# Kernel tuning notes

Measured on AMD Instinct MI355X. Metric: run time of the kernel, lower is better.

The kernel has to match this reference:

```python
import jax, jax.numpy as jnp
import numpy as np

B, T, D, U = 32, 2048, 1024, 1024

def setup_inputs() -> dict:
    key = jax.random.key(0)
    ks = jax.random.split(key, 6)
    scale = 1.0 / np.sqrt(D)
    return {
        "features": jax.random.normal(ks[0], (B, T, D), dtype=jnp.float32),
        "hidden": jax.random.normal(ks[1], (B, D), dtype=jnp.float32),
        "W1": jax.random.normal(ks[2], (D, U), dtype=jnp.float32) * scale,
        "b1": jnp.zeros((U,), dtype=jnp.float32),
        "W2": jax.random.normal(ks[3], (D, U), dtype=jnp.float32) * scale,
        "b2": jnp.zeros((U,), dtype=jnp.float32),
        "V": jax.random.normal(ks[4], (U, 1), dtype=jnp.float32) * (1.0 / np.sqrt(U)),
        "bV": jnp.zeros((1,), dtype=jnp.float32),
    }

def reference(features, hidden, W1, b1, W2, b2, V, bV):
    # features: [B,T,D], hidden: [B,D]
    proj_f = jnp.einsum('btd,du->btu', features, W1) + b1          # [B,T,U]
    proj_h = (hidden @ W2 + b2)[:, None, :]                        # [B,1,U]
    score = jnp.tanh(proj_f + proj_h)                              # [B,T,U]
    logits = jnp.einsum('btu,uo->bto', score, V) + bV              # [B,T,1]
    attention_weights = jax.nn.softmax(logits, axis=1)             # [B,T,1]
    context_vector = jnp.sum(attention_weights * features, axis=1) # [B,D]
    return context_vector, attention_weights
```

## Files before the change

### kernel.cpp

```cpp
#include <hip/hip_runtime.h>
#include <hip/hip_bf16.h>
#include <hip/hip_fp16.h>

#define B_ 32
#define T_ 2048
#define D_ 1024
#define U_ 1024
#define M_ (B_ * T_)
#define NT_ 16

typedef _Float16 f16x8 __attribute__((ext_vector_type(8)));
typedef float f32x4 __attribute__((ext_vector_type(4)));

__device__ __forceinline__ float fast_tanh(float x) {
    float xc = fminf(fmaxf(x, -10.f), 10.f);
    float e = __expf(2.f * xc);
    return 1.f - 2.f / (e + 1.f);
}

__device__ __forceinline__ void load_lds16(const void* g, void* l) {
    __builtin_amdgcn_global_load_lds(
        (const __attribute__((address_space(1))) void*)g,
        (__attribute__((address_space(3))) void*)l, 16, 0, 0);
}

__global__ void precastT_kernel(const float* __restrict__ in,
                                _Float16* __restrict__ out) {
    __shared__ __align__(16) _Float16 lds[16 * 1024];
    int mt = blockIdx.x;
    int t = threadIdx.x;
    const float* src = in + (size_t)mt * 16384;
    #pragma unroll
    for (int i = 0; i < 4; ++i) {
        int o = (i * 256 + t) * 16;
        int r = o >> 10, c = o & 1023;
        f32x4 a0 = *(const f32x4*)(src + o);
        f32x4 a1 = *(const f32x4*)(src + o + 4);
        f32x4 a2 = *(const f32x4*)(src + o + 8);
        f32x4 a3 = *(const f32x4*)(src + o + 12);
        f16x8 h0, h1;
        h0[0]=(_Float16)a0[0]; h0[1]=(_Float16)a0[1]; h0[2]=(_Float16)a0[2]; h0[3]=(_Float16)a0[3];
        h0[4]=(_Float16)a1[0]; h0[5]=(_Float16)a1[1]; h0[6]=(_Float16)a1[2]; h0[7]=(_Float16)a1[3];
        h1[0]=(_Float16)a2[0]; h1[1]=(_Float16)a2[1]; h1[2]=(_Float16)a2[2]; h1[3]=(_Float16)a2[3];
        h1[4]=(_Float16)a3[0]; h1[5]=(_Float16)a3[1]; h1[6]=(_Float16)a3[2]; h1[7]=(_Float16)a3[3];
        int u0 = c >> 3, swz = r & 7;
        *(f16x8*)((char*)lds + r * 2048 + ((u0 ^ swz) << 4)) = h0;
        *(f16x8*)((char*)lds + r * 2048 + (((u0 + 1) ^ swz) << 4)) = h1;
    }
    __syncthreads();
    int slot = t & 15, kb0 = t >> 4, ssw = slot & 7;
    _Float16* dst = out + (size_t)mt * 16384 + slot * 8;
    #pragma unroll
    for (int i = 0; i < 8; ++i) {
        int kb = kb0 + i * 16;
        f16x8 h = *(const f16x8*)((char*)lds + slot * 2048 + ((kb ^ ssw) << 4));
        *(f16x8*)(dst + kb * 128) = h;
    }
}

__global__ void transpose_cast_W1T_kernel(const float* __restrict__ W1,
                                          _Float16* __restrict__ W1T) {
    int u = blockIdx.x * 256 + threadIdx.x;
    int d0 = blockIdx.y * 64;
    _Float16* dst = W1T + (size_t)(u >> 4) * 16384 + (u & 15) * 8;
    for (int j8 = 0; j8 < 8; ++j8) {
        f16x8 h;
        #pragma unroll
        for (int j = 0; j < 8; ++j)
            h[j] = (_Float16)W1[(size_t)(d0 + j8 * 8 + j) * U_ + u];
        *(f16x8*)(dst + (size_t)(d0 / 8 + j8) * 128) = h;
    }
}

__global__ void proj_h_partial_kernel(const float* __restrict__ hidden,
                                      const float* __restrict__ W2,
                                      float* __restrict__ pph) {
    int u = blockIdx.x * 256 + threadIdx.x;
    int c = blockIdx.y;
    __shared__ float hb[32][128];
    for (int i = threadIdx.x; i < 32 * 128; i += 256)
        hb[i >> 7][i & 127] = hidden[(i >> 7) * D_ + c * 128 + (i & 127)];
    __syncthreads();
    float acc[32] = {};
    for (int d = 0; d < 128; ++d) {
        float w = W2[(size_t)(c * 128 + d) * U_ + u];
        #pragma unroll
        for (int b = 0; b < 32; ++b) acc[b] = fmaf(hb[b][d], w, acc[b]);
    }
    #pragma unroll
    for (int b = 0; b < 32; ++b)
        pph[((size_t)c * 32 + b) * U_ + u] = acc[b];
}

__global__ void proj_h_combine_kernel(const float* __restrict__ pph,
                                      const float* __restrict__ b1,
                                      const float* __restrict__ b2,
                                      float* __restrict__ ph) {
    int u = blockIdx.x * 256 + threadIdx.x;
    float bias = b1[u] + b2[u];
    for (int b = 0; b < 32; ++b) {
        float s = bias;
        #pragma unroll
        for (int c = 0; c < 8; ++c) s += pph[((size_t)c * 32 + b) * U_ + u];
        ph[b * U_ + u] = s;
    }
}


#define LOAD_AF(dst, s) do { \
    const char* a_ = aT + (s) * 1024; \
    _Pragma("unroll") \
    for (int m_ = 0; m_ < 4; ++m_) \
        dst[m_] = *(const f16x8*)(a_ + (m_ << 15)); \
} while (0)

#define READ_BF(s) do { \
    _Pragma("unroll") \
    for (int n_ = 0; n_ < 4; ++n_) \
        bfc[n_] = *(const f16x8*)(lB + n_ * 32768 + (s) * 1024 + l16); \
} while (0)

#define MFMA_STEP(AF) do { \
    __builtin_amdgcn_s_setprio(1); \
    _Pragma("unroll") \
    for (int m_ = 0; m_ < 4; ++m_) \
        _Pragma("unroll") \
        for (int n_ = 0; n_ < 4; ++n_) \
            acc[m_][n_] = __builtin_amdgcn_mfma_f32_16x16x32_f16( \
                AF[m_], bfc[n_], acc[m_][n_], 0, 0, 0); \
    __builtin_amdgcn_s_setprio(0); \
} while (0)

__global__ __launch_bounds__(1024, 4)
void gemm_logits_v8_kernel(const _Float16* __restrict__ featT,
                           const _Float16* __restrict__ W1T,
                           const float* __restrict__ ph,
                           const float* __restrict__ V,
                           float* __restrict__ part)
{
    __shared__ __align__(16) _Float16 Bs[65536];

    int bid = blockIdx.x;
    int xcd = bid & 7, local = bid >> 3;
    int nt = local & 15;
    int mg = xcd * 8 + (local >> 4);

    int tid = threadIdx.x;
    int l = tid & 63, w = tid >> 6;
    int l16 = l * 16;
    const char* lB = (const char*)Bs;

    const char* aT = (const char*)featT + ((size_t)(mg * 64 + w * 4) << 15) + l16;

    {
        const char* src = (const char*)W1T + (size_t)nt * 131072;
        #pragma unroll
        for (int i = 0; i < 8; ++i)
            load_lds16(src + i * 16384 + tid * 16, (char*)Bs + i * 16384 + tid * 16);
    }

    f16x8 afA[4], afB[4], bfc[4];
    f32x4 acc[4][4] = {};

    LOAD_AF(afA, 0);

    float Vv[4];
    #pragma unroll
    for (int n = 0; n < 4; ++n) Vv[n] = V[nt * 64 + n * 16 + (l & 15)];

    asm volatile("s_waitcnt vmcnt(0)" ::: "memory");
    __builtin_amdgcn_s_barrier();

    #pragma unroll 1
    for (int s = 0; s < 32; s += 2) {
        READ_BF(s);
        LOAD_AF(afB, s + 1);
        MFMA_STEP(afA);
        READ_BF(s + 1);
        if (s < 30) LOAD_AF(afA, s + 2);
        MFMA_STEP(afB);
    }

    int row0 = mg * 1024 + w * 64;
    const float* phb = ph + (mg >> 1) * U_;
    float phv[4];
    #pragma unroll
    for (int n = 0; n < 4; ++n) phv[n] = phb[nt * 64 + n * 16 + (l & 15)];
    #pragma unroll
    for (int m = 0; m < 4; ++m) {
        #pragma unroll
        for (int r = 0; r < 4; ++r) {
            float p = 0.f;
            #pragma unroll
            for (int n = 0; n < 4; ++n)
                p = fmaf(fast_tanh(acc[m][n][r] + phv[n]), Vv[n], p);
            p += __shfl_xor(p, 1, 64);
            p += __shfl_xor(p, 2, 64);
            p += __shfl_xor(p, 4, 64);
            p += __shfl_xor(p, 8, 64);
            if ((l & 15) == 0)
                part[(size_t)nt * M_ + row0 + m * 16 + (l >> 4) * 4 + r] = p;
        }
    }
}

__global__ void softmax_kernel(const float* __restrict__ part,
                               float* __restrict__ wout) {
    int b = blockIdx.x;
    int tid = threadIdx.x;
    __shared__ float red[8];
    float lg[8];
    #pragma unroll
    for (int j = 0; j < 8; ++j) {
        int t = tid + j * 256;
        float s = 0.f;
        #pragma unroll
        for (int p = 0; p < NT_; ++p)
            s += part[(size_t)p * M_ + b * T_ + t];
        lg[j] = s;
    }
    float mx = lg[0];
    #pragma unroll
    for (int j = 1; j < 8; ++j) mx = fmaxf(mx, lg[j]);
    #pragma unroll
    for (int off = 1; off < 64; off <<= 1) mx = fmaxf(mx, __shfl_xor(mx, off, 64));
    int wv = tid >> 6;
    if ((tid & 63) == 0) red[wv] = mx;
    __syncthreads();
    mx = fmaxf(fmaxf(red[0], red[1]), fmaxf(red[2], red[3]));
    float e[8];
    float sum = 0.f;
    #pragma unroll
    for (int j = 0; j < 8; ++j) { e[j] = __expf(lg[j] - mx); sum += e[j]; }
    #pragma unroll
    for (int off = 1; off < 64; off <<= 1) sum += __shfl_xor(sum, off, 64);
    if ((tid & 63) == 0) red[4 + wv] = sum;
    __syncthreads();
    sum = red[4] + red[5] + red[6] + red[7];
    float inv = 1.f / sum;
    #pragma unroll
    for (int j = 0; j < 8; ++j)
        wout[b * T_ + tid + j * 256] = e[j] * inv;
}

__global__ void context_v7_kernel(const _Float16* __restrict__ featT,
                                  const float* __restrict__ w,
                                  float* __restrict__ ctx) {
    int b = blockIdx.x;
    int dc = blockIdx.y;
    int t = threadIdx.x;
    __shared__ float wLds[2048];
    for (int i = t; i < 2048; i += 256) wLds[i] = w[b * T_ + i];
    __syncthreads();

    float acc[8] = {};
    const char* base = (const char*)featT + (size_t)b * 128 * 32768 + dc * 4096 + t * 16;
    int slot = t & 15;
    #pragma unroll 4
    for (int mt = 0; mt < 128; ++mt) {
        f16x8 v = *(const f16x8*)(base + (size_t)mt * 32768);
        float wt = wLds[mt * 16 + slot];
        #pragma unroll
        for (int j = 0; j < 8; ++j) acc[j] = fmaf(wt, (float)v[j], acc[j]);
    }
    #pragma unroll
    for (int j = 0; j < 8; ++j) {
        acc[j] += __shfl_xor(acc[j], 1, 64);
        acc[j] += __shfl_xor(acc[j], 2, 64);
        acc[j] += __shfl_xor(acc[j], 4, 64);
        acc[j] += __shfl_xor(acc[j], 8, 64);
    }
    if ((t & 15) == 0) {
        float* o = ctx + b * D_ + dc * 128 + (t >> 4) * 8;
        #pragma unroll
        for (int j = 0; j < 8; ++j) o[j] = acc[j];
    }
}

extern "C" void kernel_launch(void* const* d_in, const int* in_sizes, int n_in,
                              void* d_out, int out_size, void* d_ws, size_t ws_size,
                              hipStream_t stream) {
    const float* features = (const float*)d_in[0];
    const float* hidden   = (const float*)d_in[1];
    const float* W1       = (const float*)d_in[2];
    const float* b1       = (const float*)d_in[3];
    const float* W2       = (const float*)d_in[4];
    const float* b2       = (const float*)d_in[5];
    const float* V        = (const float*)d_in[6];

    float* ctx_out = (float*)d_out;
    float* w_out   = ctx_out + B_ * D_;

    char* ws = (char*)d_ws;
    _Float16* W1T  = (_Float16*)ws;
    float* ph      = (float*)(ws + (size_t)(2 << 20));
    float* pph     = (float*)(ws + (size_t)(2 << 20) + (1 << 17));
    float* part    = (float*)(ws + (size_t)(4 << 20));
    _Float16* featT = (_Float16*)(ws + (size_t)(8 << 20));

    transpose_cast_W1T_kernel<<<dim3(4, 16), 256, 0, stream>>>(W1, W1T);
    proj_h_partial_kernel<<<dim3(4, 8), 256, 0, stream>>>(hidden, W2, pph);
    proj_h_combine_kernel<<<4, 256, 0, stream>>>(pph, b1, b2, ph);
    precastT_kernel<<<4096, 256, 0, stream>>>(features, featT);

    gemm_logits_v8_kernel<<<1024, 1024, 0, stream>>>(featT, W1T, ph, V, part);

    softmax_kernel<<<B_, 256, 0, stream>>>(part, w_out);
    context_v7_kernel<<<dim3(B_, 8), 256, 0, stream>>>(featT, w_out, ctx_out);
}
```

Before: 314.8 us.

## Switch logits GEMM to 32x32x16 MFMA with matching 32-row pre-swizzled layouts

Replaces the 16x16x32 MFMA tiling with 32x32x16 MFMA instructions, so each wave computes a 64x64 tile with 2x2 larger accumulators. The feature and W1 precast kernels are rewritten to emit a 32-row interleaved fp16 layout that the new fragment loads expect, and the context kernel is adapted to that layout. The main loop now double-buffers both A and B fragments and adds sched_barriers to fix the interleaving of loads and MFMAs. The intent is fewer MFMA issues and fewer fragment loads per FLOP. The cost is larger per-lane accumulator state, a changed epilogue reduction, and context-kernel access patterns that may be less efficient.

```diff
diff --git a/kernel.cpp b/kernel.cpp
--- a/kernel.cpp
+++ b/kernel.cpp
@@ -11,6 +11,7 @@
 
 typedef _Float16 f16x8 __attribute__((ext_vector_type(8)));
 typedef float f32x4 __attribute__((ext_vector_type(4)));
+typedef float f32x16 __attribute__((ext_vector_type(16)));
 
 __device__ __forceinline__ float fast_tanh(float x) {
     float xc = fminf(fmaxf(x, -10.f), 10.f);
@@ -26,35 +27,33 @@
 
 __global__ void precastT_kernel(const float* __restrict__ in,
                                 _Float16* __restrict__ out) {
-    __shared__ __align__(16) _Float16 lds[16 * 1024];
+    __shared__ __align__(16) _Float16 lds[32 * 1024];
     int mt = blockIdx.x;
     int t = threadIdx.x;
-    const float* src = in + (size_t)mt * 16384;
-    #pragma unroll
-    for (int i = 0; i < 4; ++i) {
-        int o = (i * 256 + t) * 16;
-        int r = o >> 10, c = o & 1023;
-        f32x4 a0 = *(const f32x4*)(src + o);
-        f32x4 a1 = *(const f32x4*)(src + o + 4);
-        f32x4 a2 = *(const f32x4*)(src + o + 8);
-        f32x4 a3 = *(const f32x4*)(src + o + 12);
-        f16x8 h0, h1;
-        h0[0]=(_Float16)a0[0]; h0[1]=(_Float16)a0[1]; h0[2]=(_Float16)a0[2]; h0[3]=(_Float16)a0[3];
-        h0[4]=(_Float16)a1[0]; h0[5]=(_Float16)a1[1]; h0[6]=(_Float16)a1[2]; h0[7]=(_Float16)a1[3];
-        h1[0]=(_Float16)a2[0]; h1[1]=(_Float16)a2[1]; h1[2]=(_Float16)a2[2]; h1[3]=(_Float16)a2[3];
-        h1[4]=(_Float16)a3[0]; h1[5]=(_Float16)a3[1]; h1[6]=(_Float16)a3[2]; h1[7]=(_Float16)a3[3];
-        int u0 = c >> 3, swz = r & 7;
-        *(f16x8*)((char*)lds + r * 2048 + ((u0 ^ swz) << 4)) = h0;
-        *(f16x8*)((char*)lds + r * 2048 + (((u0 + 1) ^ swz) << 4)) = h1;
-    }
-    __syncthreads();
-    int slot = t & 15, kb0 = t >> 4, ssw = slot & 7;
-    _Float16* dst = out + (size_t)mt * 16384 + slot * 8;
-    #pragma unroll
-    for (int i = 0; i < 8; ++i) {
-        int kb = kb0 + i * 16;
-        f16x8 h = *(const f16x8*)((char*)lds + slot * 2048 + ((kb ^ ssw) << 4));
-        *(f16x8*)(dst + kb * 128) = h;
+    const float* src = in + (size_t)mt * 32 * 1024;
+    #pragma unroll
+    for (int i = 0; i < 16; ++i) {
+        int idx = (i * 256 + t) * 8;
+        int row = idx >> 10, k = idx & 1023;
+        f32x4 a = *(const f32x4*)(src + idx);
+        f32x4 b = *(const f32x4*)(src + idx + 4);
+        f16x8 h;
+        h[0]=(_Float16)a[0]; h[1]=(_Float16)a[1]; h[2]=(_Float16)a[2]; h[3]=(_Float16)a[3];
+        h[4]=(_Float16)b[0]; h[5]=(_Float16)b[1]; h[6]=(_Float16)b[2]; h[7]=(_Float16)b[3];
+        int u = k >> 3;
+        *(f16x8*)((char*)lds + row * 2048 + ((u ^ (row & 15)) << 4)) = h;
+    }
+    __syncthreads();
+    char* dst = (char*)out + (size_t)mt * 65536;
+    #pragma unroll
+    for (int i = 0; i < 16; ++i) {
+        int o = i * 4096 + t * 16;
+        int k16 = o >> 10;
+        int l = (o >> 4) & 63;
+        int row = l & 31, khalf = l >> 5;
+        int u = k16 * 2 + khalf;
+        f16x8 h = *(const f16x8*)((char*)lds + row * 2048 + ((u ^ (row & 15)) << 4));
+        *(f16x8*)(dst + o) = h;
     }
 }
 
@@ -62,13 +61,15 @@
                                           _Float16* __restrict__ W1T) {
     int u = blockIdx.x * 256 + threadIdx.x;
     int d0 = blockIdx.y * 64;
-    _Float16* dst = W1T + (size_t)(u >> 4) * 16384 + (u & 15) * 8;
+    char* base = (char*)W1T + (size_t)(u >> 5) * 65536 + (u & 31) * 16;
     for (int j8 = 0; j8 < 8; ++j8) {
+        int k = d0 + j8 * 8;
         f16x8 h;
         #pragma unroll
         for (int j = 0; j < 8; ++j)
-            h[j] = (_Float16)W1[(size_t)(d0 + j8 * 8 + j) * U_ + u];
-        *(f16x8*)(dst + (size_t)(d0 / 8 + j8) * 128) = h;
+            h[j] = (_Float16)W1[(size_t)(k + j) * U_ + u];
+        int k16 = k >> 4, khalf = (k >> 3) & 1;
+        *(f16x8*)(base + k16 * 1024 + khalf * 512) = h;
     }
 }
 
@@ -107,33 +108,30 @@
 }
 
 
-#define LOAD_AF(dst, s) do { \
-    const char* a_ = aT + (s) * 1024; \
-    _Pragma("unroll") \
-    for (int m_ = 0; m_ < 4; ++m_) \
-        dst[m_] = *(const f16x8*)(a_ + (m_ << 15)); \
+#define SB0 __builtin_amdgcn_sched_barrier(0);
+
+#define LOAD_AF(dst, s16) do { \
+    dst[0] = *(const f16x8*)(aT + (s16) * 1024); \
+    dst[1] = *(const f16x8*)(aT + 65536 + (s16) * 1024); \
 } while (0)
 
-#define READ_BF(s) do { \
-    _Pragma("unroll") \
-    for (int n_ = 0; n_ < 4; ++n_) \
-        bfc[n_] = *(const f16x8*)(lB + n_ * 32768 + (s) * 1024 + l16); \
+#define READ_BF(dst, s16) do { \
+    dst[0] = *(const f16x8*)(lB + (s16) * 1024 + l16); \
+    dst[1] = *(const f16x8*)(lB + 65536 + (s16) * 1024 + l16); \
 } while (0)
 
-#define MFMA_STEP(AF) do { \
+#define MFMA4(AF, BF) do { \
     __builtin_amdgcn_s_setprio(1); \
-    _Pragma("unroll") \
-    for (int m_ = 0; m_ < 4; ++m_) \
-        _Pragma("unroll") \
-        for (int n_ = 0; n_ < 4; ++n_) \
-            acc[m_][n_] = __builtin_amdgcn_mfma_f32_16x16x32_f16( \
-                AF[m_], bfc[n_], acc[m_][n_], 0, 0, 0); \
+    acc[0][0] = __builtin_amdgcn_mfma_f32_32x32x16_f16(AF[0], BF[0], acc[0][0], 0, 0, 0); \
+    acc[0][1] = __builtin_amdgcn_mfma_f32_32x32x16_f16(AF[0], BF[1], acc[0][1], 0, 0, 0); \
+    acc[1][0] = __builtin_amdgcn_mfma_f32_32x32x16_f16(AF[1], BF[0], acc[1][0], 0, 0, 0); \
+    acc[1][1] = __builtin_amdgcn_mfma_f32_32x32x16_f16(AF[1], BF[1], acc[1][1], 0, 0, 0); \
     __builtin_amdgcn_s_setprio(0); \
 } while (0)
 
 __global__ __launch_bounds__(1024, 4)
-void gemm_logits_v8_kernel(const _Float16* __restrict__ featT,
-                           const _Float16* __restrict__ W1T,
+void gemm_logits_v9_kernel(const _Float16* __restrict__ featT2,
+                           const _Float16* __restrict__ W1T2,
                            const float* __restrict__ ph,
                            const float* __restrict__ V,
                            float* __restrict__ part)
@@ -148,58 +146,69 @@
     int tid = threadIdx.x;
     int l = tid & 63, w = tid >> 6;
     int l16 = l * 16;
+    int l31 = l & 31, hi = l >> 5;
     const char* lB = (const char*)Bs;
 
-    const char* aT = (const char*)featT + ((size_t)(mg * 64 + w * 4) << 15) + l16;
-
     {
-        const char* src = (const char*)W1T + (size_t)nt * 131072;
+        const char* src = (const char*)W1T2 + (size_t)nt * 131072;
         #pragma unroll
         for (int i = 0; i < 8; ++i)
             load_lds16(src + i * 16384 + tid * 16, (char*)Bs + i * 16384 + tid * 16);
     }
 
-    f16x8 afA[4], afB[4], bfc[4];
-    f32x4 acc[4][4] = {};
+    const char* aT = (const char*)featT2 + ((size_t)(mg * 32 + w * 2) << 16) + l16;
+
+    f16x8 afA[2], afB[2], bfA[2], bfB[2];
+    f32x16 acc[2][2] = {};
 
     LOAD_AF(afA, 0);
 
-    float Vv[4];
-    #pragma unroll
-    for (int n = 0; n < 4; ++n) Vv[n] = V[nt * 64 + n * 16 + (l & 15)];
+    float Vv[2], phv[2];
+    const float* phb = ph + (mg >> 1) * U_;
+    #pragma unroll
+    for (int n = 0; n < 2; ++n) {
+        int u = nt * 64 + n * 32 + l31;
+        Vv[n] = V[u];
+        phv[n] = phb[u];
+    }
 
     asm volatile("s_waitcnt vmcnt(0)" ::: "memory");
     __builtin_amdgcn_s_barrier();
 
+    READ_BF(bfA, 0);
+
     #pragma unroll 1
-    for (int s = 0; s < 32; s += 2) {
-        READ_BF(s);
+    for (int s = 0; s < 64; s += 2) {
         LOAD_AF(afB, s + 1);
-        MFMA_STEP(afA);
-        READ_BF(s + 1);
-        if (s < 30) LOAD_AF(afA, s + 2);
-        MFMA_STEP(afB);
+        READ_BF(bfB, s + 1);
+        SB0
+        MFMA4(afA, bfA);
+        SB0
+        if (s < 62) {
+            LOAD_AF(afA, s + 2);
+            READ_BF(bfA, s + 2);
+        }
+        SB0
+        MFMA4(afB, bfB);
+        SB0
     }
 
     int row0 = mg * 1024 + w * 64;
-    const float* phb = ph + (mg >> 1) * U_;
-    float phv[4];
-    #pragma unroll
-    for (int n = 0; n < 4; ++n) phv[n] = phb[nt * 64 + n * 16 + (l & 15)];
-    #pragma unroll
-    for (int m = 0; m < 4; ++m) {
-        #pragma unroll
-        for (int r = 0; r < 4; ++r) {
-            float p = 0.f;
-            #pragma unroll
-            for (int n = 0; n < 4; ++n)
-                p = fmaf(fast_tanh(acc[m][n][r] + phv[n]), Vv[n], p);
+    #pragma unroll
+    for (int m = 0; m < 2; ++m) {
+        #pragma unroll
+        for (int reg = 0; reg < 16; ++reg) {
+            float p = fmaf(fast_tanh(acc[m][0][reg] + phv[0]), Vv[0],
+                           fast_tanh(acc[m][1][reg] + phv[1]) * Vv[1]);
             p += __shfl_xor(p, 1, 64);
             p += __shfl_xor(p, 2, 64);
             p += __shfl_xor(p, 4, 64);
             p += __shfl_xor(p, 8, 64);
-            if ((l & 15) == 0)
-                part[(size_t)nt * M_ + row0 + m * 16 + (l >> 4) * 4 + r] = p;
+            p += __shfl_xor(p, 16, 64);
+            if (l31 == 0) {
+                int row = row0 + m * 32 + (reg & 3) + 8 * (reg >> 2) + 4 * hi;
+                part[(size_t)nt * M_ + row] = p;
+            }
         }
     }
 }
@@ -243,7 +252,7 @@
         wout[b * T_ + tid + j * 256] = e[j] * inv;
 }
 
-__global__ void context_v7_kernel(const _Float16* __restrict__ featT,
+__global__ void context_v8_kernel(const _Float16* __restrict__ featT2,
                                   const float* __restrict__ w,
                                   float* __restrict__ ctx) {
     int b = blockIdx.x;
@@ -253,27 +262,34 @@
     for (int i = t; i < 2048; i += 256) wLds[i] = w[b * T_ + i];
     __syncthreads();
 
-    float acc[8] = {};
-    const char* base = (const char*)featT + (size_t)b * 128 * 32768 + dc * 4096 + t * 16;
-    int slot = t & 15;
-    #pragma unroll 4
-    for (int mt = 0; mt < 128; ++mt) {
-        f16x8 v = *(const f16x8*)(base + (size_t)mt * 32768);
-        float wt = wLds[mt * 16 + slot];
-        #pragma unroll
-        for (int j = 0; j < 8; ++j) acc[j] = fmaf(wt, (float)v[j], acc[j]);
-    }
-    #pragma unroll
-    for (int j = 0; j < 8; ++j) {
-        acc[j] += __shfl_xor(acc[j], 1, 64);
-        acc[j] += __shfl_xor(acc[j], 2, 64);
-        acc[j] += __shfl_xor(acc[j], 4, 64);
-        acc[j] += __shfl_xor(acc[j], 8, 64);
-    }
-    if ((t & 15) == 0) {
-        float* o = ctx + b * D_ + dc * 128 + (t >> 4) * 8;
-        #pragma unroll
-        for (int j = 0; j < 8; ++j) o[j] = acc[j];
+    int l = t & 63, g = t >> 6;
+    int row = l & 31, khalf = l >> 5;
+    #pragma unroll
+    for (int pass = 0; pass < 2; ++pass) {
+        int k16 = dc * 8 + pass * 4 + g;
+        const char* base = (const char*)featT2 + ((size_t)(b * 64) << 16)
+                         + k16 * 1024 + l * 16;
+        float acc[8] = {};
+        #pragma unroll 4
+        for (int mt = 0; mt < 64; ++mt) {
+            f16x8 v = *(const f16x8*)(base + ((size_t)mt << 16));
+            float wt = wLds[mt * 32 + row];
+            #pragma unroll
+            for (int j = 0; j < 8; ++j) acc[j] = fmaf(wt, (float)v[j], acc[j]);
+        }
+        #pragma unroll
+        for (int j = 0; j < 8; ++j) {
+            acc[j] += __shfl_xor(acc[j], 1, 64);
+            acc[j] += __shfl_xor(acc[j], 2, 64);
+            acc[j] += __shfl_xor(acc[j], 4, 64);
+            acc[j] += __shfl_xor(acc[j], 8, 64);
+            acc[j] += __shfl_xor(acc[j], 16, 64);
+        }
+        if (row == 0) {
+            float* o = ctx + b * D_ + k16 * 16 + khalf * 8;
+            #pragma unroll
+            for (int j = 0; j < 8; ++j) o[j] = acc[j];
+        }
     }
 }
 
@@ -301,10 +317,10 @@
     transpose_cast_W1T_kernel<<<dim3(4, 16), 256, 0, stream>>>(W1, W1T);
     proj_h_partial_kernel<<<dim3(4, 8), 256, 0, stream>>>(hidden, W2, pph);
     proj_h_combine_kernel<<<4, 256, 0, stream>>>(pph, b1, b2, ph);
-    precastT_kernel<<<4096, 256, 0, stream>>>(features, featT);
-
-    gemm_logits_v8_kernel<<<1024, 1024, 0, stream>>>(featT, W1T, ph, V, part);
+    precastT_kernel<<<2048, 256, 0, stream>>>(features, featT);
+
+    gemm_logits_v9_kernel<<<1024, 1024, 0, stream>>>(featT, W1T, ph, V, part);
 
     softmax_kernel<<<B_, 256, 0, stream>>>(part, w_out);
-    context_v7_kernel<<<dim3(B_, 8), 256, 0, stream>>>(featT, w_out, ctx_out);
-}
+    context_v8_kernel<<<dim3(B_, 8), 256, 0, stream>>>(featT, w_out, ctx_out);
+}
```

After: 352.8 us. +12.1%, slower.

## Make GEMM-logits kernel persistent, looping over eight M chunks per resident W1 tile

Applied to the files above, without the earlier changes.

The fused GEMM+tanh+V kernel is relaunched with 256 blocks instead of 1024. Each block loads its 64-column W1 tile into LDS once and then loops over eight 512-row chunks of features, with a smaller 2x4 MFMA tile per wave. The inner loop now double-buffers B fragments from LDS and prefetches the next chunk's A fragments across chunk boundaries. This cuts repeated W1 LDS fills and launch tail effects, but gives less parallelism per launch and a smaller per-wave tile.

```diff
diff --git a/kernel.cpp b/kernel.cpp
--- a/kernel.cpp
+++ b/kernel.cpp
@@ -107,50 +107,47 @@
 }
 
 
-#define LOAD_AF(dst, s) do { \
-    const char* a_ = aT + (s) * 1024; \
-    _Pragma("unroll") \
-    for (int m_ = 0; m_ < 4; ++m_) \
-        dst[m_] = *(const f16x8*)(a_ + (m_ << 15)); \
-} while (0)
-
-#define READ_BF(s) do { \
-    _Pragma("unroll") \
-    for (int n_ = 0; n_ < 4; ++n_) \
-        bfc[n_] = *(const f16x8*)(lB + n_ * 32768 + (s) * 1024 + l16); \
-} while (0)
-
-#define MFMA_STEP(AF) do { \
+#define MFMA8(AF, BF) do { \
     __builtin_amdgcn_s_setprio(1); \
     _Pragma("unroll") \
-    for (int m_ = 0; m_ < 4; ++m_) \
+    for (int m_ = 0; m_ < 2; ++m_) \
         _Pragma("unroll") \
         for (int n_ = 0; n_ < 4; ++n_) \
             acc[m_][n_] = __builtin_amdgcn_mfma_f32_16x16x32_f16( \
-                AF[m_], bfc[n_], acc[m_][n_], 0, 0, 0); \
+                AF[m_], BF[n_], acc[m_][n_], 0, 0, 0); \
     __builtin_amdgcn_s_setprio(0); \
 } while (0)
 
+#define LOAD_AF(dst, base, s) do { \
+    dst[0] = *(const f16x8*)((base) + (s) * 1024); \
+    dst[1] = *(const f16x8*)((base) + 32768 + (s) * 1024); \
+} while (0)
+
+#define READ_BF(dst, s) do { \
+    _Pragma("unroll") \
+    for (int n_ = 0; n_ < 4; ++n_) \
+        dst[n_] = *(const f16x8*)(lB + n_ * 32768 + (s) * 1024 + l16); \
+} while (0)
+
 __global__ __launch_bounds__(1024, 4)
-void gemm_logits_v8_kernel(const _Float16* __restrict__ featT,
-                           const _Float16* __restrict__ W1T,
-                           const float* __restrict__ ph,
-                           const float* __restrict__ V,
-                           float* __restrict__ part)
+void gemm_logits_v10_kernel(const _Float16* __restrict__ featT,
+                            const _Float16* __restrict__ W1T,
+                            const float* __restrict__ ph,
+                            const float* __restrict__ V,
+                            float* __restrict__ part)
 {
     __shared__ __align__(16) _Float16 Bs[65536];
 
     int bid = blockIdx.x;
-    int xcd = bid & 7, local = bid >> 3;
-    int nt = local & 15;
-    int mg = xcd * 8 + (local >> 4);
+    int xcd = bid & 7, cu = bid >> 3;
+    int nt = cu & 15, half = cu >> 4;
+    int mgp0 = xcd * 16 + half * 8;
 
     int tid = threadIdx.x;
     int l = tid & 63, w = tid >> 6;
     int l16 = l * 16;
     const char* lB = (const char*)Bs;
-
-    const char* aT = (const char*)featT + ((size_t)(mg * 64 + w * 4) << 15) + l16;
+    const char* fT = (const char*)featT;
 
     {
         const char* src = (const char*)W1T + (size_t)nt * 131072;
@@ -159,48 +156,63 @@
             load_lds16(src + i * 16384 + tid * 16, (char*)Bs + i * 16384 + tid * 16);
     }
 
-    f16x8 afA[4], afB[4], bfc[4];
-    f32x4 acc[4][4] = {};
-
-    LOAD_AF(afA, 0);
-
     float Vv[4];
     #pragma unroll
     for (int n = 0; n < 4; ++n) Vv[n] = V[nt * 64 + n * 16 + (l & 15)];
+
+    f16x8 afA[2], afB[2], bfA[4], bfB[4];
+    f32x4 acc[2][4] = {};
+
+    const char* aCur = fT + ((size_t)((mgp0 * 32) + w * 2) << 15) + l16;
+    LOAD_AF(afA, aCur, 0);
 
     asm volatile("s_waitcnt vmcnt(0)" ::: "memory");
     __builtin_amdgcn_s_barrier();
 
+    READ_BF(bfA, 0);
+
     #pragma unroll 1
-    for (int s = 0; s < 32; s += 2) {
-        READ_BF(s);
-        LOAD_AF(afB, s + 1);
-        MFMA_STEP(afA);
-        READ_BF(s + 1);
-        if (s < 30) LOAD_AF(afA, s + 2);
-        MFMA_STEP(afB);
-    }
-
-    int row0 = mg * 1024 + w * 64;
-    const float* phb = ph + (mg >> 1) * U_;
-    float phv[4];
-    #pragma unroll
-    for (int n = 0; n < 4; ++n) phv[n] = phb[nt * 64 + n * 16 + (l & 15)];
-    #pragma unroll
-    for (int m = 0; m < 4; ++m) {
-        #pragma unroll
-        for (int r = 0; r < 4; ++r) {
-            float p = 0.f;
+    for (int c = 0; c < 8; ++c) {
+        const char* aNext = fT + ((size_t)(((mgp0 + (c < 7 ? c + 1 : c)) * 32) + w * 2) << 15) + l16;
+
+        #pragma unroll 1
+        for (int s = 0; s < 32; s += 2) {
+            LOAD_AF(afB, aCur, s + 1);
+            READ_BF(bfB, s + 1);
+            MFMA8(afA, bfA);
+            if (s < 30) LOAD_AF(afA, aCur, s + 2);
+            else        LOAD_AF(afA, aNext, 0);
+            READ_BF(bfA, (s + 2) & 31);
+            MFMA8(afB, bfB);
+        }
+
+        int row0 = (mgp0 + c) * 512 + w * 32;
+        const float* phb = ph + ((mgp0 + c) >> 2) * U_;
+        float phv[4];
+        #pragma unroll
+        for (int n = 0; n < 4; ++n) phv[n] = phb[nt * 64 + n * 16 + (l & 15)];
+        #pragma unroll
+        for (int m = 0; m < 2; ++m) {
+            #pragma unroll
+            for (int r = 0; r < 4; ++r) {
+                float p = 0.f;
+                #pragma unroll
+                for (int n = 0; n < 4; ++n)
+                    p = fmaf(fast_tanh(acc[m][n][r] + phv[n]), Vv[n], p);
+                p += __shfl_xor(p, 1, 64);
+                p += __shfl_xor(p, 2, 64);
+                p += __shfl_xor(p, 4, 64);
+                p += __shfl_xor(p, 8, 64);
+                if ((l & 15) == 0)
+                    part[(size_t)nt * M_ + row0 + m * 16 + (l >> 4) * 4 + r] = p;
+            }
+        }
+        #pragma unroll
+        for (int m = 0; m < 2; ++m)
             #pragma unroll
             for (int n = 0; n < 4; ++n)
-                p = fmaf(fast_tanh(acc[m][n][r] + phv[n]), Vv[n], p);
-            p += __shfl_xor(p, 1, 64);
-            p += __shfl_xor(p, 2, 64);
-            p += __shfl_xor(p, 4, 64);
-            p += __shfl_xor(p, 8, 64);
-            if ((l & 15) == 0)
-                part[(size_t)nt * M_ + row0 + m * 16 + (l >> 4) * 4 + r] = p;
-        }
+                acc[m][n] = (f32x4){0.f, 0.f, 0.f, 0.f};
+        aCur = aNext;
     }
 }
 
@@ -303,7 +315,7 @@
     proj_h_combine_kernel<<<4, 256, 0, stream>>>(pph, b1, b2, ph);
     precastT_kernel<<<4096, 256, 0, stream>>>(features, featT);
 
-    gemm_logits_v8_kernel<<<1024, 1024, 0, stream>>>(featT, W1T, ph, V, part);
+    gemm_logits_v10_kernel<<<256, 1024, 0, stream>>>(featT, W1T, ph, V, part);
 
     softmax_kernel<<<B_, 256, 0, stream>>>(part, w_out);
     context_v7_kernel<<<dim3(B_, 8), 256, 0, stream>>>(featT, w_out, ctx_out);
```

Measured after the change: 314.5 us. About the same (-0.1%).
